# Performance work log

Measured on AMD Instinct MI355X. Metric: run time of the kernel, lower is better.

The kernel has to match this reference:

```python
import jax, jax.numpy as jnp
import numpy as np

# Fixed causal graph: 32 endo nodes, each with a private 16-dim exogenous parent.
# Nodes 0..3 are roots (no endo parents); node i>=4 has endo parents {i-4..i-1}.
N_NODES = 32
ENDO = 16      # endogenous features per node
EXO = 16       # exogenous features per node
HID = 64       # hidden width (module default hidden_features=[64,64])
N_ROOTS = 4
N_PAR = 4      # endo parents for non-root nodes
IN_ROOT = EXO                      # 16
IN_INNER = N_PAR * ENDO + EXO      # 80
BATCH = 32768


def _init(key, shape, fan_in):
    return jax.random.normal(key, shape, jnp.float32) * (1.0 / np.sqrt(fan_in))


def setup_inputs() -> dict:
    key = jax.random.key(0)
    ks = jax.random.split(key, 13)
    n_in = N_NODES - N_ROOTS
    return {
        "u": jax.random.normal(ks[0], (BATCH, N_NODES * EXO), jnp.float32),
        # stacked root MLPs: [n_roots, in, out]
        "w_r1": _init(ks[1], (N_ROOTS, IN_ROOT, HID), IN_ROOT),
        "b_r1": jnp.zeros((N_ROOTS, HID), jnp.float32),
        "w_r2": _init(ks[2], (N_ROOTS, HID, HID), HID),
        "b_r2": jnp.zeros((N_ROOTS, HID), jnp.float32),
        "w_r3": _init(ks[3], (N_ROOTS, HID, ENDO), HID),
        "b_r3": jnp.zeros((N_ROOTS, ENDO), jnp.float32),
        # stacked inner MLPs: [n_inner, in, out]
        "w_i1": _init(ks[4], (n_in, IN_INNER, HID), IN_INNER),
        "b_i1": jnp.zeros((n_in, HID), jnp.float32),
        "w_i2": _init(ks[5], (n_in, HID, HID), HID),
        "b_i2": jnp.zeros((n_in, HID), jnp.float32),
        "w_i3": _init(ks[6], (n_in, HID, ENDO), HID),
        "b_i3": jnp.zeros((n_in, ENDO), jnp.float32),
    }


def _mlp(x, w1, b1, w2, b2, w3, b3):
    h = jax.nn.relu(x @ w1 + b1)
    h = jax.nn.relu(h @ w2 + b2)
    return h @ w3 + b3


def reference(u, w_r1, b_r1, w_r2, b_r2, w_r3, b_r3,
              w_i1, b_i1, w_i2, b_i2, w_i3, b_i3):
    B = u.shape[0]
    U = u.reshape(B, N_NODES, EXO)  # per-node exogenous inputs
    # Root nodes: no endo parents, vectorized over the 4 roots.
    h = jax.nn.relu(jnp.einsum("bni,nio->bno", U[:, :N_ROOTS], w_r1) + b_r1)
    h = jax.nn.relu(jnp.einsum("bnh,nho->bno", h, w_r2) + b_r2)
    root_v = jnp.einsum("bnh,nhd->bnd", h, w_r3) + b_r3  # [B, 4, ENDO]
    V = [root_v[:, i] for i in range(N_ROOTS)]
    # Non-root nodes in topological order: gather thresholded parents -> MLP.
    for i in range(N_ROOTS, N_NODES):
        j = i - N_ROOTS
        parents = jnp.concatenate(
            [(V[p] > 0.5).astype(u.dtype) for p in range(i - N_PAR, i)], axis=-1)
        inp = jnp.concatenate([parents, U[:, i]], axis=-1)  # [B, 80]
        V.append(_mlp(inp, w_i1[j], b_i1[j], w_i2[j], b_i2[j], w_i3[j], b_i3[j]))
    # forward() uses soft=True, T/W_T/W_E=None -> E is the raw logits, batched.
    return jnp.concatenate(V, axis=-1)  # [B, N_NODES*ENDO]
```

## Files before the change

### kernel.cpp

```cpp
#include <hip/hip_runtime.h>


#define BT 64

typedef __attribute__((ext_vector_type(8))) short bf16x8;
typedef __attribute__((ext_vector_type(4))) float f32x4;
#define MFMA16 __builtin_amdgcn_mfma_f32_16x16x32_bf16

#define NODE_STRIDE 33792
#define W1_SPLIT    6144
#define W2_OFF      18432
#define W2_SPLIT    4096
#define W3_OFF      30720
#define W3_SPLIT    1024

__device__ inline unsigned short bf16_rne(float x) {
    unsigned u = __float_as_uint(x);
    u += 0x7fffu + ((u >> 16) & 1u);
    return (unsigned short)(u >> 16);
}
__device__ inline float bf16_tof(unsigned short h) {
    return __uint_as_float(((unsigned)h) << 16);
}
__device__ inline void split3(float x, unsigned short& h, unsigned short& m,
                              unsigned short& l) {
    h = bf16_rne(x);
    float r = x - bf16_tof(h);
    m = bf16_rne(r);
    float r2 = r - bf16_tof(m);
    l = bf16_rne(r2);
}

#define PER_NODE_ITEMS (64 * 96 + 64 * 64 + 16 * 64)

__global__ void prep_weights(const float* __restrict__ w_r1,
                             const float* __restrict__ w_r2,
                             const float* __restrict__ w_r3,
                             const float* __restrict__ w_i1,
                             const float* __restrict__ w_i2,
                             const float* __restrict__ w_i3,
                             unsigned short* __restrict__ ws) {
    int tid = blockIdx.x * 256 + threadIdx.x;
    if (tid >= 32 * PER_NODE_ITEMS) return;
    int node = tid / PER_NODE_ITEMS;
    int r = tid - node * PER_NODE_ITEMS;
    int off, stride;
    float wv = 0.0f;
    if (r < 6144) {
        int n = r / 96, k = r - n * 96;
        if (k < 64) {
            wv = (node >= 4) ? w_i1[((node - 4) * 80 + k) * 64 + n] : 0.0f;
        } else if (k < 80) {
            wv = (node < 4) ? w_r1[(node * 16 + (k - 64)) * 64 + n]
                            : w_i1[((node - 4) * 80 + k) * 64 + n];
        }
        off = n * 96 + k; stride = W1_SPLIT;
    } else if (r < 10240) {
        int r2 = r - 6144;
        int n = r2 >> 6, k = r2 & 63;
        wv = (node < 4) ? w_r2[(node * 64 + k) * 64 + n]
                        : w_i2[((node - 4) * 64 + k) * 64 + n];
        off = W2_OFF + n * 64 + k; stride = W2_SPLIT;
    } else {
        int r3 = r - 10240;
        int n = r3 >> 6, k = r3 & 63;
        wv = (node < 4) ? w_r3[(node * 64 + k) * 16 + n]
                        : w_i3[((node - 4) * 64 + k) * 16 + n];
        off = W3_OFF + n * 64 + k; stride = W3_SPLIT;
    }
    unsigned short h, m, l;
    split3(wv, h, m, l);
    unsigned short* base = ws + node * NODE_STRIDE;
    base[off] = h;
    base[off + stride] = m;
    base[off + 2 * stride] = l;
}

__global__ __launch_bounds__(256, 2) void ncm_mfma(
    const float* __restrict__ u,
    const unsigned short* __restrict__ ws,
    const float* __restrict__ b_r1, const float* __restrict__ b_r2,
    const float* __restrict__ b_r3, const float* __restrict__ b_i1,
    const float* __restrict__ b_i2, const float* __restrict__ b_i3,
    float* __restrict__ out)
{
    __shared__ __align__(16) unsigned short ring[4][64][24];
    __shared__ __align__(16) unsigned short xu[3][64][32];
    __shared__ __align__(16) unsigned short h1s[3][64][72];
    __shared__ __align__(16) unsigned short h2s[3][64][72];

    const int tid = threadIdx.x;
    const int l   = tid & 63;
    const int w   = tid >> 6;
    const int lr  = l & 15;
    const int lq  = l >> 4;

    for (int z = tid; z < 4 * 64 * 24; z += 256) ((unsigned short*)ring)[z] = 0;
    for (int z = tid; z < 3 * 64 * 32; z += 256) ((unsigned short*)xu)[z] = 0;

    const long eg = (long)blockIdx.x * BT;
    const float* u_blk = u + eg * 512;
    const int n1 = 16 * w + lr;

    for (int i = 0; i < 32; ++i) {
        __syncthreads();

        float4 uv = *(const float4*)(u_blk + (long)l * 512 + i * 16 + w * 4);
        {
            unsigned short h0, m0, l0, h1, m1, l1, h2, m2, l2, h3, m3, l3;
            split3(uv.x, h0, m0, l0); split3(uv.y, h1, m1, l1);
            split3(uv.z, h2, m2, l2); split3(uv.w, h3, m3, l3);
            ushort4 vh = make_ushort4(h0, h1, h2, h3);
            ushort4 vm = make_ushort4(m0, m1, m2, m3);
            ushort4 vl = make_ushort4(l0, l1, l2, l3);
            *(ushort4*)&xu[0][l][4 * w] = vh;
            *(ushort4*)&xu[1][l][4 * w] = vm;
            *(ushort4*)&xu[2][l][4 * w] = vl;
        }
        __syncthreads();

        const unsigned short* Wn = ws + i * NODE_STRIDE;

        f32x4 acc[4] = {{0,0,0,0},{0,0,0,0},{0,0,0,0},{0,0,0,0}};
        {
            if (i >= 4) {
                #pragma unroll
                for (int k0 = 0; k0 < 64; k0 += 32) {
                    const int f = k0 + lq * 8;
                    const int slot = (i + (f >> 4)) & 3;
                    bf16x8 wb0 = *(const bf16x8*)(Wn + 0 * W1_SPLIT + n1 * 96 + f);
                    bf16x8 wb1 = *(const bf16x8*)(Wn + 1 * W1_SPLIT + n1 * 96 + f);
                    bf16x8 wb2 = *(const bf16x8*)(Wn + 2 * W1_SPLIT + n1 * 96 + f);
                    #pragma unroll
                    for (int m = 0; m < 4; ++m) {
                        bf16x8 ab = *(const bf16x8*)&ring[slot][m * 16 + lr][f & 15];
                        acc[m] = MFMA16(ab, wb0, acc[m], 0, 0, 0);
                        acc[m] = MFMA16(ab, wb1, acc[m], 0, 0, 0);
                        acc[m] = MFMA16(ab, wb2, acc[m], 0, 0, 0);
                    }
                }
            }
            {
                const int f = lq * 8;
                bf16x8 wb0 = *(const bf16x8*)(Wn + 0 * W1_SPLIT + n1 * 96 + 64 + f);
                bf16x8 wb1 = *(const bf16x8*)(Wn + 1 * W1_SPLIT + n1 * 96 + 64 + f);
                bf16x8 wb2 = *(const bf16x8*)(Wn + 2 * W1_SPLIT + n1 * 96 + 64 + f);
                #pragma unroll
                for (int m = 0; m < 4; ++m) {
                    const int e = m * 16 + lr;
                    bf16x8 a0 = *(const bf16x8*)&xu[0][e][f];
                    bf16x8 a1 = *(const bf16x8*)&xu[1][e][f];
                    bf16x8 a2 = *(const bf16x8*)&xu[2][e][f];
                    acc[m] = MFMA16(a0, wb0, acc[m], 0, 0, 0);
                    acc[m] = MFMA16(a0, wb1, acc[m], 0, 0, 0);
                    acc[m] = MFMA16(a0, wb2, acc[m], 0, 0, 0);
                    acc[m] = MFMA16(a1, wb0, acc[m], 0, 0, 0);
                    acc[m] = MFMA16(a1, wb1, acc[m], 0, 0, 0);
                    acc[m] = MFMA16(a1, wb2, acc[m], 0, 0, 0);
                    acc[m] = MFMA16(a2, wb0, acc[m], 0, 0, 0);
                    acc[m] = MFMA16(a2, wb1, acc[m], 0, 0, 0);
                }
            }
            const float b1 = (i < 4) ? b_r1[i * 64 + n1] : b_i1[(i - 4) * 64 + n1];
            #pragma unroll
            for (int m = 0; m < 4; ++m) {
                #pragma unroll
                for (int r = 0; r < 4; ++r) {
                    const int e = m * 16 + lq * 4 + r;
                    float v = fmaxf(acc[m][r] + b1, 0.0f);
                    unsigned short sh, sm, sl;
                    split3(v, sh, sm, sl);
                    h1s[0][e][n1] = sh; h1s[1][e][n1] = sm; h1s[2][e][n1] = sl;
                }
            }
        }
        __syncthreads();

        {
            #pragma unroll
            for (int m = 0; m < 4; ++m) acc[m] = (f32x4){0,0,0,0};
            const unsigned short* W2 = Wn + W2_OFF;
            #pragma unroll
            for (int k0 = 0; k0 < 64; k0 += 32) {
                const int f = k0 + lq * 8;
                bf16x8 wb0 = *(const bf16x8*)(W2 + 0 * W2_SPLIT + n1 * 64 + f);
                bf16x8 wb1 = *(const bf16x8*)(W2 + 1 * W2_SPLIT + n1 * 64 + f);
                bf16x8 wb2 = *(const bf16x8*)(W2 + 2 * W2_SPLIT + n1 * 64 + f);
                #pragma unroll
                for (int m = 0; m < 4; ++m) {
                    const int e = m * 16 + lr;
                    bf16x8 a0 = *(const bf16x8*)&h1s[0][e][f];
                    bf16x8 a1 = *(const bf16x8*)&h1s[1][e][f];
                    bf16x8 a2 = *(const bf16x8*)&h1s[2][e][f];
                    acc[m] = MFMA16(a0, wb0, acc[m], 0, 0, 0);
                    acc[m] = MFMA16(a0, wb1, acc[m], 0, 0, 0);
                    acc[m] = MFMA16(a0, wb2, acc[m], 0, 0, 0);
                    acc[m] = MFMA16(a1, wb0, acc[m], 0, 0, 0);
                    acc[m] = MFMA16(a1, wb1, acc[m], 0, 0, 0);
                    acc[m] = MFMA16(a1, wb2, acc[m], 0, 0, 0);
                    acc[m] = MFMA16(a2, wb0, acc[m], 0, 0, 0);
                    acc[m] = MFMA16(a2, wb1, acc[m], 0, 0, 0);
                }
            }
            const float b2 = (i < 4) ? b_r2[i * 64 + n1] : b_i2[(i - 4) * 64 + n1];
            #pragma unroll
            for (int m = 0; m < 4; ++m) {
                #pragma unroll
                for (int r = 0; r < 4; ++r) {
                    const int e = m * 16 + lq * 4 + r;
                    float v = fmaxf(acc[m][r] + b2, 0.0f);
                    unsigned short sh, sm, sl;
                    split3(v, sh, sm, sl);
                    h2s[0][e][n1] = sh; h2s[1][e][n1] = sm; h2s[2][e][n1] = sl;
                }
            }
        }
        __syncthreads();

        {
            f32x4 c3 = {0,0,0,0};
            const unsigned short* W3 = Wn + W3_OFF;
            #pragma unroll
            for (int k0 = 0; k0 < 64; k0 += 32) {
                const int f = k0 + lq * 8;
                bf16x8 wb0 = *(const bf16x8*)(W3 + 0 * W3_SPLIT + lr * 64 + f);
                bf16x8 wb1 = *(const bf16x8*)(W3 + 1 * W3_SPLIT + lr * 64 + f);
                bf16x8 wb2 = *(const bf16x8*)(W3 + 2 * W3_SPLIT + lr * 64 + f);
                const int e = 16 * w + lr;
                bf16x8 a0 = *(const bf16x8*)&h2s[0][e][f];
                bf16x8 a1 = *(const bf16x8*)&h2s[1][e][f];
                bf16x8 a2 = *(const bf16x8*)&h2s[2][e][f];
                c3 = MFMA16(a0, wb0, c3, 0, 0, 0);
                c3 = MFMA16(a0, wb1, c3, 0, 0, 0);
                c3 = MFMA16(a0, wb2, c3, 0, 0, 0);
                c3 = MFMA16(a1, wb0, c3, 0, 0, 0);
                c3 = MFMA16(a1, wb1, c3, 0, 0, 0);
                c3 = MFMA16(a1, wb2, c3, 0, 0, 0);
                c3 = MFMA16(a2, wb0, c3, 0, 0, 0);
                c3 = MFMA16(a2, wb1, c3, 0, 0, 0);
            }
            const float b3 = (i < 4) ? b_r3[i * 16 + lr] : b_i3[(i - 4) * 16 + lr];
            const int slot = i & 3;
            #pragma unroll
            for (int r = 0; r < 4; ++r) {
                const int e = 16 * w + lq * 4 + r;
                float v = c3[r] + b3;
                out[(eg + e) * 512 + i * 16 + lr] = v;
                ring[slot][e][lr] = (v > 0.5f) ? (unsigned short)0x3F80 : (unsigned short)0;
            }
        }
    }
}

extern "C" void kernel_launch(void* const* d_in, const int* in_sizes, int n_in,
                              void* d_out, int out_size, void* d_ws, size_t ws_size,
                              hipStream_t stream) {
    const float* u    = (const float*)d_in[0];
    const float* w_r1 = (const float*)d_in[1];
    const float* b_r1 = (const float*)d_in[2];
    const float* w_r2 = (const float*)d_in[3];
    const float* b_r2 = (const float*)d_in[4];
    const float* w_r3 = (const float*)d_in[5];
    const float* b_r3 = (const float*)d_in[6];
    const float* w_i1 = (const float*)d_in[7];
    const float* b_i1 = (const float*)d_in[8];
    const float* w_i2 = (const float*)d_in[9];
    const float* b_i2 = (const float*)d_in[10];
    const float* w_i3 = (const float*)d_in[11];
    const float* b_i3 = (const float*)d_in[12];
    float* out = (float*)d_out;
    unsigned short* ws = (unsigned short*)d_ws;

    prep_weights<<<dim3((32 * PER_NODE_ITEMS) / 256), dim3(256), 0, stream>>>(
        w_r1, w_r2, w_r3, w_i1, w_i2, w_i3, ws);

    ncm_mfma<<<dim3(512), dim3(256), 0, stream>>>(
        u, ws, b_r1, b_r2, b_r3, b_i1, b_i2, b_i3, out);
}
```

Before: 334.6 us.

## Split MLP work across eight waves with transposed MFMA and register-fed inputs

```diff
diff --git a/kernel.cpp b/kernel.cpp
--- a/kernel.cpp
+++ b/kernel.cpp
@@ -1,7 +1,5 @@
 #include <hip/hip_runtime.h>
 
-
-#define BT 64
 
 typedef __attribute__((ext_vector_type(8))) short bf16x8;
 typedef __attribute__((ext_vector_type(4))) float f32x4;
@@ -76,7 +74,7 @@
     base[off + 2 * stride] = l;
 }
 
-__global__ __launch_bounds__(256, 2) void ncm_mfma(
+__global__ __launch_bounds__(512, 4) void ncm_mfma(
     const float* __restrict__ u,
     const unsigned short* __restrict__ ws,
     const float* __restrict__ b_r1, const float* __restrict__ b_r2,
@@ -85,169 +83,194 @@
     float* __restrict__ out)
 {
     __shared__ __align__(16) unsigned short ring[4][64][24];
-    __shared__ __align__(16) unsigned short xu[3][64][32];
-    __shared__ __align__(16) unsigned short h1s[3][64][72];
-    __shared__ __align__(16) unsigned short h2s[3][64][72];
+    __shared__ __align__(16) unsigned short h[3][64][72];
 
     const int tid = threadIdx.x;
     const int l   = tid & 63;
     const int w   = tid >> 6;
     const int lr  = l & 15;
     const int lq  = l >> 4;
-
-    for (int z = tid; z < 4 * 64 * 24; z += 256) ((unsigned short*)ring)[z] = 0;
-    for (int z = tid; z < 3 * 64 * 32; z += 256) ((unsigned short*)xu)[z] = 0;
-
-    const long eg = (long)blockIdx.x * BT;
-    const float* u_blk = u + eg * 512;
-    const int n1 = 16 * w + lr;
+    const int n0  = (w & 3) * 16;
+    const int m0  = (w >> 2) * 2;
+    const long eg = (long)blockIdx.x * 64;
 
     for (int i = 0; i < 32; ++i) {
         __syncthreads();
 
-        float4 uv = *(const float4*)(u_blk + (long)l * 512 + i * 16 + w * 4);
+        const unsigned short* Wn = ws + i * NODE_STRIDE;
+        const int nr = n0 + lr;
+
+        float4 ua[2], ub[2];
+        if (lq < 2) {
+            #pragma unroll
+            for (int mm = 0; mm < 2; ++mm) {
+                const float* up = u + (eg + (m0 + mm) * 16 + lr) * 512 + i * 16 + lq * 8;
+                ua[mm] = *(const float4*)up;
+                ub[mm] = *(const float4*)(up + 4);
+            }
+        }
+
+        f32x4 acc[2] = {{0,0,0,0},{0,0,0,0}};
         {
-            unsigned short h0, m0, l0, h1, m1, l1, h2, m2, l2, h3, m3, l3;
-            split3(uv.x, h0, m0, l0); split3(uv.y, h1, m1, l1);
-            split3(uv.z, h2, m2, l2); split3(uv.w, h3, m3, l3);
-            ushort4 vh = make_ushort4(h0, h1, h2, h3);
-            ushort4 vm = make_ushort4(m0, m1, m2, m3);
-            ushort4 vl = make_ushort4(l0, l1, l2, l3);
-            *(ushort4*)&xu[0][l][4 * w] = vh;
-            *(ushort4*)&xu[1][l][4 * w] = vm;
-            *(ushort4*)&xu[2][l][4 * w] = vl;
-        }
-        __syncthreads();
-
-        const unsigned short* Wn = ws + i * NODE_STRIDE;
-
-        f32x4 acc[4] = {{0,0,0,0},{0,0,0,0},{0,0,0,0},{0,0,0,0}};
-        {
+            bf16x8 wa[3][3];
+            #pragma unroll
+            for (int kb = 0; kb < 3; ++kb)
+                #pragma unroll
+                for (int s = 0; s < 3; ++s)
+                    wa[kb][s] = *(const bf16x8*)(Wn + s * W1_SPLIT + nr * 96 + kb * 32 + lq * 8);
+
             if (i >= 4) {
                 #pragma unroll
-                for (int k0 = 0; k0 < 64; k0 += 32) {
-                    const int f = k0 + lq * 8;
-                    const int slot = (i + (f >> 4)) & 3;
-                    bf16x8 wb0 = *(const bf16x8*)(Wn + 0 * W1_SPLIT + n1 * 96 + f);
-                    bf16x8 wb1 = *(const bf16x8*)(Wn + 1 * W1_SPLIT + n1 * 96 + f);
-                    bf16x8 wb2 = *(const bf16x8*)(Wn + 2 * W1_SPLIT + n1 * 96 + f);
+                for (int kb = 0; kb < 2; ++kb) {
+                    const int k = kb * 32 + lq * 8;
+                    const int slot = (i + (k >> 4)) & 3;
                     #pragma unroll
-                    for (int m = 0; m < 4; ++m) {
-                        bf16x8 ab = *(const bf16x8*)&ring[slot][m * 16 + lr][f & 15];
-                        acc[m] = MFMA16(ab, wb0, acc[m], 0, 0, 0);
-                        acc[m] = MFMA16(ab, wb1, acc[m], 0, 0, 0);
-                        acc[m] = MFMA16(ab, wb2, acc[m], 0, 0, 0);
+                    for (int mm = 0; mm < 2; ++mm) {
+                        bf16x8 bits = *(const bf16x8*)&ring[slot][(m0 + mm) * 16 + lr][k & 15];
+                        acc[mm] = MFMA16(wa[kb][0], bits, acc[mm], 0, 0, 0);
+                        acc[mm] = MFMA16(wa[kb][1], bits, acc[mm], 0, 0, 0);
+                        acc[mm] = MFMA16(wa[kb][2], bits, acc[mm], 0, 0, 0);
                     }
                 }
             }
-            {
-                const int f = lq * 8;
-                bf16x8 wb0 = *(const bf16x8*)(Wn + 0 * W1_SPLIT + n1 * 96 + 64 + f);
-                bf16x8 wb1 = *(const bf16x8*)(Wn + 1 * W1_SPLIT + n1 * 96 + 64 + f);
-                bf16x8 wb2 = *(const bf16x8*)(Wn + 2 * W1_SPLIT + n1 * 96 + 64 + f);
-                #pragma unroll
-                for (int m = 0; m < 4; ++m) {
-                    const int e = m * 16 + lr;
-                    bf16x8 a0 = *(const bf16x8*)&xu[0][e][f];
-                    bf16x8 a1 = *(const bf16x8*)&xu[1][e][f];
-                    bf16x8 a2 = *(const bf16x8*)&xu[2][e][f];
-                    acc[m] = MFMA16(a0, wb0, acc[m], 0, 0, 0);
-                    acc[m] = MFMA16(a0, wb1, acc[m], 0, 0, 0);
-                    acc[m] = MFMA16(a0, wb2, acc[m], 0, 0, 0);
-                    acc[m] = MFMA16(a1, wb0, acc[m], 0, 0, 0);
-                    acc[m] = MFMA16(a1, wb1, acc[m], 0, 0, 0);
-                    acc[m] = MFMA16(a1, wb2, acc[m], 0, 0, 0);
-                    acc[m] = MFMA16(a2, wb0, acc[m], 0, 0, 0);
-                    acc[m] = MFMA16(a2, wb1, acc[m], 0, 0, 0);
-                }
-            }
-            const float b1 = (i < 4) ? b_r1[i * 64 + n1] : b_i1[(i - 4) * 64 + n1];
-            #pragma unroll
-            for (int m = 0; m < 4; ++m) {
+            bf16x8 xh[2] = {}, xm[2] = {}, xl[2] = {};
+            if (lq < 2) {
+                #pragma unroll
+                for (int mm = 0; mm < 2; ++mm) {
+                    float f[8] = {ua[mm].x, ua[mm].y, ua[mm].z, ua[mm].w,
+                                  ub[mm].x, ub[mm].y, ub[mm].z, ub[mm].w};
+                    #pragma unroll
+                    for (int j = 0; j < 8; ++j) {
+                        unsigned short sh, sm, sl;
+                        split3(f[j], sh, sm, sl);
+                        xh[mm][j] = (short)sh; xm[mm][j] = (short)sm; xl[mm][j] = (short)sl;
+                    }
+                }
+            }
+            #pragma unroll
+            for (int mm = 0; mm < 2; ++mm) {
+                acc[mm] = MFMA16(wa[2][0], xh[mm], acc[mm], 0, 0, 0);
+                acc[mm] = MFMA16(wa[2][1], xh[mm], acc[mm], 0, 0, 0);
+                acc[mm] = MFMA16(wa[2][2], xh[mm], acc[mm], 0, 0, 0);
+                acc[mm] = MFMA16(wa[2][0], xm[mm], acc[mm], 0, 0, 0);
+                acc[mm] = MFMA16(wa[2][1], xm[mm], acc[mm], 0, 0, 0);
+                acc[mm] = MFMA16(wa[2][2], xm[mm], acc[mm], 0, 0, 0);
+                acc[mm] = MFMA16(wa[2][0], xl[mm], acc[mm], 0, 0, 0);
+                acc[mm] = MFMA16(wa[2][1], xl[mm], acc[mm], 0, 0, 0);
+            }
+            const float* b1p = (i < 4) ? (b_r1 + i * 64) : (b_i1 + (i - 4) * 64);
+            float4 bv = *(const float4*)(b1p + n0 + lq * 4);
+            float bb[4] = {bv.x, bv.y, bv.z, bv.w};
+            #pragma unroll
+            for (int mm = 0; mm < 2; ++mm) {
+                const int e = (m0 + mm) * 16 + lr;
+                unsigned long long ph = 0, pm = 0, pl = 0;
                 #pragma unroll
                 for (int r = 0; r < 4; ++r) {
-                    const int e = m * 16 + lq * 4 + r;
-                    float v = fmaxf(acc[m][r] + b1, 0.0f);
+                    float v = fmaxf(acc[mm][r] + bb[r], 0.0f);
                     unsigned short sh, sm, sl;
                     split3(v, sh, sm, sl);
-                    h1s[0][e][n1] = sh; h1s[1][e][n1] = sm; h1s[2][e][n1] = sl;
-                }
+                    ph |= ((unsigned long long)sh) << (16 * r);
+                    pm |= ((unsigned long long)sm) << (16 * r);
+                    pl |= ((unsigned long long)sl) << (16 * r);
+                }
+                *(unsigned long long*)&h[0][e][n0 + lq * 4] = ph;
+                *(unsigned long long*)&h[1][e][n0 + lq * 4] = pm;
+                *(unsigned long long*)&h[2][e][n0 + lq * 4] = pl;
             }
         }
         __syncthreads();
 
         {
-            #pragma unroll
-            for (int m = 0; m < 4; ++m) acc[m] = (f32x4){0,0,0,0};
-            const unsigned short* W2 = Wn + W2_OFF;
-            #pragma unroll
-            for (int k0 = 0; k0 < 64; k0 += 32) {
-                const int f = k0 + lq * 8;
-                bf16x8 wb0 = *(const bf16x8*)(W2 + 0 * W2_SPLIT + n1 * 64 + f);
-                bf16x8 wb1 = *(const bf16x8*)(W2 + 1 * W2_SPLIT + n1 * 64 + f);
-                bf16x8 wb2 = *(const bf16x8*)(W2 + 2 * W2_SPLIT + n1 * 64 + f);
-                #pragma unroll
-                for (int m = 0; m < 4; ++m) {
-                    const int e = m * 16 + lr;
-                    bf16x8 a0 = *(const bf16x8*)&h1s[0][e][f];
-                    bf16x8 a1 = *(const bf16x8*)&h1s[1][e][f];
-                    bf16x8 a2 = *(const bf16x8*)&h1s[2][e][f];
-                    acc[m] = MFMA16(a0, wb0, acc[m], 0, 0, 0);
-                    acc[m] = MFMA16(a0, wb1, acc[m], 0, 0, 0);
-                    acc[m] = MFMA16(a0, wb2, acc[m], 0, 0, 0);
-                    acc[m] = MFMA16(a1, wb0, acc[m], 0, 0, 0);
-                    acc[m] = MFMA16(a1, wb1, acc[m], 0, 0, 0);
-                    acc[m] = MFMA16(a1, wb2, acc[m], 0, 0, 0);
-                    acc[m] = MFMA16(a2, wb0, acc[m], 0, 0, 0);
-                    acc[m] = MFMA16(a2, wb1, acc[m], 0, 0, 0);
-                }
-            }
-            const float b2 = (i < 4) ? b_r2[i * 64 + n1] : b_i2[(i - 4) * 64 + n1];
-            #pragma unroll
-            for (int m = 0; m < 4; ++m) {
+            bf16x8 wa[2][3];
+            #pragma unroll
+            for (int kb = 0; kb < 2; ++kb)
+                #pragma unroll
+                for (int s = 0; s < 3; ++s)
+                    wa[kb][s] = *(const bf16x8*)(Wn + W2_OFF + s * W2_SPLIT + nr * 64 + kb * 32 + lq * 8);
+            f32x4 acc2[2] = {{0,0,0,0},{0,0,0,0}};
+            #pragma unroll
+            for (int kb = 0; kb < 2; ++kb) {
+                const int ko = kb * 32 + lq * 8;
+                #pragma unroll
+                for (int mm = 0; mm < 2; ++mm) {
+                    const int e = (m0 + mm) * 16 + lr;
+                    bf16x8 a0 = *(const bf16x8*)&h[0][e][ko];
+                    bf16x8 a1 = *(const bf16x8*)&h[1][e][ko];
+                    bf16x8 a2 = *(const bf16x8*)&h[2][e][ko];
+                    acc2[mm] = MFMA16(wa[kb][0], a0, acc2[mm], 0, 0, 0);
+                    acc2[mm] = MFMA16(wa[kb][1], a0, acc2[mm], 0, 0, 0);
+                    acc2[mm] = MFMA16(wa[kb][2], a0, acc2[mm], 0, 0, 0);
+                    acc2[mm] = MFMA16(wa[kb][0], a1, acc2[mm], 0, 0, 0);
+                    acc2[mm] = MFMA16(wa[kb][1], a1, acc2[mm], 0, 0, 0);
+                    acc2[mm] = MFMA16(wa[kb][2], a1, acc2[mm], 0, 0, 0);
+                    acc2[mm] = MFMA16(wa[kb][0], a2, acc2[mm], 0, 0, 0);
+                    acc2[mm] = MFMA16(wa[kb][1], a2, acc2[mm], 0, 0, 0);
+                }
+            }
+            __syncthreads();
+            const float* b2p = (i < 4) ? (b_r2 + i * 64) : (b_i2 + (i - 4) * 64);
+            float4 bv = *(const float4*)(b2p + n0 + lq * 4);
+            float bb[4] = {bv.x, bv.y, bv.z, bv.w};
+            #pragma unroll
+            for (int mm = 0; mm < 2; ++mm) {
+                const int e = (m0 + mm) * 16 + lr;
+                unsigned long long ph = 0, pm = 0, pl = 0;
                 #pragma unroll
                 for (int r = 0; r < 4; ++r) {
-                    const int e = m * 16 + lq * 4 + r;
-                    float v = fmaxf(acc[m][r] + b2, 0.0f);
+                    float v = fmaxf(acc2[mm][r] + bb[r], 0.0f);
                     unsigned short sh, sm, sl;
                     split3(v, sh, sm, sl);
-                    h2s[0][e][n1] = sh; h2s[1][e][n1] = sm; h2s[2][e][n1] = sl;
-                }
+                    ph |= ((unsigned long long)sh) << (16 * r);
+                    pm |= ((unsigned long long)sm) << (16 * r);
+                    pl |= ((unsigned long long)sl) << (16 * r);
+                }
+                *(unsigned long long*)&h[0][e][n0 + lq * 4] = ph;
+                *(unsigned long long*)&h[1][e][n0 + lq * 4] = pm;
+                *(unsigned long long*)&h[2][e][n0 + lq * 4] = pl;
             }
         }
         __syncthreads();
 
-        {
+        if ((w & 1) == 0) {
+            const int t = w >> 1;
+            const int e = t * 16 + lr;
+            bf16x8 wa[2][3];
+            #pragma unroll
+            for (int kb = 0; kb < 2; ++kb)
+                #pragma unroll
+                for (int s = 0; s < 3; ++s)
+                    wa[kb][s] = *(const bf16x8*)(Wn + W3_OFF + s * W3_SPLIT + lr * 64 + kb * 32 + lq * 8);
             f32x4 c3 = {0,0,0,0};
-            const unsigned short* W3 = Wn + W3_OFF;
-            #pragma unroll
-            for (int k0 = 0; k0 < 64; k0 += 32) {
-                const int f = k0 + lq * 8;
-                bf16x8 wb0 = *(const bf16x8*)(W3 + 0 * W3_SPLIT + lr * 64 + f);
-                bf16x8 wb1 = *(const bf16x8*)(W3 + 1 * W3_SPLIT + lr * 64 + f);
-                bf16x8 wb2 = *(const bf16x8*)(W3 + 2 * W3_SPLIT + lr * 64 + f);
-                const int e = 16 * w + lr;
-                bf16x8 a0 = *(const bf16x8*)&h2s[0][e][f];
-                bf16x8 a1 = *(const bf16x8*)&h2s[1][e][f];
-                bf16x8 a2 = *(const bf16x8*)&h2s[2][e][f];
-                c3 = MFMA16(a0, wb0, c3, 0, 0, 0);
-                c3 = MFMA16(a0, wb1, c3, 0, 0, 0);
-                c3 = MFMA16(a0, wb2, c3, 0, 0, 0);
-                c3 = MFMA16(a1, wb0, c3, 0, 0, 0);
-                c3 = MFMA16(a1, wb1, c3, 0, 0, 0);
-                c3 = MFMA16(a1, wb2, c3, 0, 0, 0);
-                c3 = MFMA16(a2, wb0, c3, 0, 0, 0);
-                c3 = MFMA16(a2, wb1, c3, 0, 0, 0);
-            }
-            const float b3 = (i < 4) ? b_r3[i * 16 + lr] : b_i3[(i - 4) * 16 + lr];
-            const int slot = i & 3;
+            #pragma unroll
+            for (int kb = 0; kb < 2; ++kb) {
+                const int ko = kb * 32 + lq * 8;
+                bf16x8 a0 = *(const bf16x8*)&h[0][e][ko];
+                bf16x8 a1 = *(const bf16x8*)&h[1][e][ko];
+                bf16x8 a2 = *(const bf16x8*)&h[2][e][ko];
+                c3 = MFMA16(wa[kb][0], a0, c3, 0, 0, 0);
+                c3 = MFMA16(wa[kb][1], a0, c3, 0, 0, 0);
+                c3 = MFMA16(wa[kb][2], a0, c3, 0, 0, 0);
+                c3 = MFMA16(wa[kb][0], a1, c3, 0, 0, 0);
+                c3 = MFMA16(wa[kb][1], a1, c3, 0, 0, 0);
+                c3 = MFMA16(wa[kb][2], a1, c3, 0, 0, 0);
+                c3 = MFMA16(wa[kb][0], a2, c3, 0, 0, 0);
+                c3 = MFMA16(wa[kb][1], a2, c3, 0, 0, 0);
+            }
+            const float* b3p = (i < 4) ? (b_r3 + i * 16) : (b_i3 + (i - 4) * 16);
+            float4 bv = *(const float4*)(b3p + lq * 4);
+            float bb[4] = {bv.x, bv.y, bv.z, bv.w};
+            float4 vo;
+            unsigned long long pbits = 0;
+            float vr[4];
             #pragma unroll
             for (int r = 0; r < 4; ++r) {
-                const int e = 16 * w + lq * 4 + r;
-                float v = c3[r] + b3;
-                out[(eg + e) * 512 + i * 16 + lr] = v;
-                ring[slot][e][lr] = (v > 0.5f) ? (unsigned short)0x3F80 : (unsigned short)0;
-            }
+                vr[r] = c3[r] + bb[r];
+                pbits |= ((unsigned long long)(vr[r] > 0.5f ? 0x3F80u : 0u)) << (16 * r);
+            }
+            vo.x = vr[0]; vo.y = vr[1]; vo.z = vr[2]; vo.w = vr[3];
+            *(float4*)(out + (eg + e) * 512 + i * 16 + lq * 4) = vo;
+            *(unsigned long long*)&ring[i & 3][e][lq * 4] = pbits;
         }
     }
 }
@@ -274,6 +297,6 @@
     prep_weights<<<dim3((32 * PER_NODE_ITEMS) / 256), dim3(256), 0, stream>>>(
         w_r1, w_r2, w_r3, w_i1, w_i2, w_i3, ws);
 
-    ncm_mfma<<<dim3(512), dim3(256), 0, stream>>>(
+    ncm_mfma<<<dim3(512), dim3(512), 0, stream>>>(
         u, ws, b_r1, b_r2, b_r3, b_i1, b_i2, b_i3, out);
 }
```

Result: slower. 438.4 us (+31.0%).
